# Kernel optimization log

Hardware: AMD Instinct MI355X
Metric: run time of the kernel (lower is better)

## Reference

```python
import jax, jax.numpy as jnp
import numpy as np

B, T, C, H = 4, 4096, 2048, 128  # batch, seq, emb_dim, head_size


def setup_inputs() -> dict:
    key = jax.random.key(0)
    k1, k2, k3, k4 = jax.random.split(key, 4)
    idx = jax.random.normal(k1, (B, T, C), dtype=jnp.float32)
    # nn.Linear weight layout: [out_features, in_features]; scale like torch init
    s = 1.0 / np.sqrt(C)
    Wq = jax.random.uniform(k2, (H, C), jnp.float32, -s, s)
    Wk = jax.random.uniform(k3, (H, C), jnp.float32, -s, s)
    Wv = jax.random.uniform(k4, (H, C), jnp.float32, -s, s)
    return {"idx": idx, "Wq": Wq, "Wk": Wk, "Wv": Wv}


def reference(idx, Wq, Wk, Wv):
    b, t, c = idx.shape
    q = jnp.einsum('btc,hc->bth', idx, Wq)  # [B,T,H]
    k = jnp.einsum('btc,hc->bth', idx, Wk)
    v = jnp.einsum('btc,hc->bth', idx, Wv)
    # NOTE: original computes keys @ queries^T and scales by emb_dim**-0.5
    scale = jnp.asarray(c, idx.dtype) ** -0.5
    wei = jnp.einsum('bih,bjh->bij', k, q) * scale  # [B,T,T]
    causal = jnp.tril(jnp.ones((t, t), dtype=bool))
    wei = jnp.where(causal, wei, -jnp.inf)
    wei = jax.nn.softmax(wei, axis=-1)
    return jnp.einsum('bij,bjh->bih', wei, v)  # [B,T,H]
```

## Files before the change

kernel.cpp:

```cpp
#include <hip/hip_runtime.h>
#include <hip/hip_bf16.h>
#include <cstdint>

#define TSEQ 4096
#define CDIM 2048
#define HDIM 128
#define NCOL 384

typedef short bf8v __attribute__((ext_vector_type(8)));
typedef float f4v  __attribute__((ext_vector_type(4)));

__device__ __forceinline__ unsigned short f2b(float f) {
  union { float f; unsigned u; } v; v.f = f;
  unsigned u = v.u;
  return (unsigned short)((u + 0x7fffu + ((u >> 16) & 1u)) >> 16);
}

__device__ __forceinline__ f4v mfma16(bf8v a, bf8v b, f4v c) {
  return __builtin_amdgcn_mfma_f32_16x16x32_bf16(a, b, c, 0, 0, 0);
}

__global__ void wcat_kernel(const float* __restrict__ Wq, const float* __restrict__ Wk,
                            const float* __restrict__ Wv, unsigned short* __restrict__ Wcat) {
  int e = (blockIdx.x * 256 + threadIdx.x) * 4;
  int n = e >> 11;
  int k = e & 2047;
  const float* src;
  if (n < 128)      src = Wq + (size_t)n * CDIM + k;
  else if (n < 256) src = Wk + (size_t)(n - 128) * CDIM + k;
  else              src = Wv + (size_t)(n - 256) * CDIM + k;
  float4 f = *(const float4*)src;
  ushort4 o;
  o.x = f2b(f.x); o.y = f2b(f.y); o.z = f2b(f.z); o.w = f2b(f.w);
  *(ushort4*)(Wcat + e) = o;
}

__global__ __launch_bounds__(256, 2) void proj_gemm(const float* __restrict__ A,
                                                    const unsigned short* __restrict__ Bw,
                                                    unsigned short* __restrict__ Cq) {
  __shared__ unsigned short As[128][40];
  __shared__ unsigned short Bs[128][40];
  const int m0 = blockIdx.x * 128;
  const int n0 = blockIdx.y * 128;
  const int tid = threadIdx.x;
  const int lane = tid & 63;
  const int w = tid >> 6;
  const int wm = (w & 1) * 64, wn = (w >> 1) * 64;
  const int llo = lane & 15, lhi = lane >> 4;

  f4v acc[4][4];
#pragma unroll
  for (int i = 0; i < 4; ++i)
#pragma unroll
    for (int j = 0; j < 4; ++j) acc[i][j] = (f4v){0.f, 0.f, 0.f, 0.f};

  const int ar = tid >> 3, ac = (tid & 7) * 4;
  const int br = tid >> 2, bc = (tid & 3) * 8;

  for (int k0 = 0; k0 < CDIM; k0 += 32) {
#pragma unroll
    for (int p = 0; p < 4; ++p) {
      int row = p * 32 + ar;
      float4 f = *(const float4*)(A + (size_t)(m0 + row) * CDIM + k0 + ac);
      ushort4 o;
      o.x = f2b(f.x); o.y = f2b(f.y); o.z = f2b(f.z); o.w = f2b(f.w);
      *(ushort4*)&As[row][ac] = o;
    }
#pragma unroll
    for (int p = 0; p < 2; ++p) {
      int row = p * 64 + br;
      *(uint4*)&Bs[row][bc] = *(const uint4*)(Bw + (size_t)(n0 + row) * CDIM + k0 + bc);
    }
    __syncthreads();
    bf8v af[4], bfr[4];
#pragma unroll
    for (int i = 0; i < 4; ++i) af[i]  = *(const bf8v*)&As[wm + i * 16 + llo][lhi * 8];
#pragma unroll
    for (int j = 0; j < 4; ++j) bfr[j] = *(const bf8v*)&Bs[wn + j * 16 + llo][lhi * 8];
#pragma unroll
    for (int i = 0; i < 4; ++i)
#pragma unroll
      for (int j = 0; j < 4; ++j) acc[i][j] = mfma16(af[i], bfr[j], acc[i][j]);
    __syncthreads();
  }
#pragma unroll
  for (int i = 0; i < 4; ++i)
#pragma unroll
    for (int j = 0; j < 4; ++j)
#pragma unroll
      for (int r = 0; r < 4; ++r) {
        int row = m0 + wm + i * 16 + lhi * 4 + r;
        int col = n0 + wn + j * 16 + llo;
        Cq[(size_t)row * NCOL + col] = f2b(acc[i][j][r]);
      }
}

__global__ void pack_frags(const unsigned short* __restrict__ qkv,
                           unsigned short* __restrict__ dst, int colbase) {
  int x = blockIdx.x;
  int b = x >> 8, t16 = x & 255;
  int t = threadIdx.x;
  int kk = t >> 6, lhi = (t >> 4) & 3, llo = t & 15;
  size_t row = (size_t)(b * TSEQ + t16 * 16 + llo);
  bf8v v = *(const bf8v*)(qkv + row * NCOL + colbase + kk * 32 + lhi * 8);
  *(bf8v*)(dst + ((size_t)x * 256 + t) * 8) = v;
}

__global__ void pack_vb(const unsigned short* __restrict__ qkv,
                        unsigned short* __restrict__ VB) {
  __shared__ unsigned short tile[64][136];
  int x = blockIdx.x;
  int b = x >> 6, j64 = x & 63;
  int t = threadIdx.x;
  {
    int r = t >> 2, c = (t & 3) * 32;
    const unsigned short* src = qkv + (size_t)(b * TSEQ + j64 * 64 + r) * NCOL + 256 + c;
    *(uint4*)&tile[r][c]      = *(const uint4*)(src);
    *(uint4*)&tile[r][c + 8]  = *(const uint4*)(src + 8);
    *(uint4*)&tile[r][c + 16] = *(const uint4*)(src + 16);
    *(uint4*)&tile[r][c + 24] = *(const uint4*)(src + 24);
  }
  __syncthreads();
#pragma unroll
  for (int p = 0; p < 4; ++p) {
    int ss = p * 256 + t;
    int jb = ss >> 9, ht = (ss >> 6) & 7, lane = ss & 63;
    int llo = lane & 15, lhi = lane >> 4;
    bf8v v;
#pragma unroll
    for (int e = 0; e < 8; ++e) v[e] = (short)tile[jb * 32 + lhi * 8 + e][ht * 16 + llo];
    *(bf8v*)(VB + (((size_t)(b * 128 + j64 * 2 + jb) * 8 + ht) * 64 + lane) * 8) = v;
  }
}

__global__ __launch_bounds__(256, 4) void attn2(const unsigned short* __restrict__ QB,
                                                const unsigned short* __restrict__ KA,
                                                const unsigned short* __restrict__ VB,
                                                float* __restrict__ out) {
  __shared__ union SM {
    unsigned short Ps[4][16][68];
    struct { float Om[4][16][132]; float Mm[4][16]; float Lm[4][16]; } mg;
  } sm;
  const int x = blockIdx.x;
  const int pair = x >> 1, member = x & 1;
  const int b = pair & 3, sp = pair >> 2;
  const int s = member ? (255 - sp) : sp;
  const int lastjt = s >> 2;
  const int tid = threadIdx.x;
  const int w = tid >> 6, lane = tid & 63;
  const int llo = lane & 15, lhi = lane >> 4;
  const float scale = 0.022097086912079608f;

  bf8v aK[4];
  {
    const unsigned short* kp = KA + (size_t)(b * 256 + s) * 2048;
#pragma unroll
    for (int kk = 0; kk < 4; ++kk) aK[kk] = *(const bf8v*)(kp + (kk * 64 + lane) * 8);
  }

  f4v Oacc[8];
#pragma unroll
  for (int nt = 0; nt < 8; ++nt) Oacc[nt] = (f4v){0.f, 0.f, 0.f, 0.f};
  float mrow[4] = {-3.0e38f, -3.0e38f, -3.0e38f, -3.0e38f};
  float lrow[4] = {0.f, 0.f, 0.f, 0.f};

  for (int jt = w; jt <= lastjt; jt += 4) {
    const unsigned short* qp = QB + (size_t)(b * 256 + jt * 4) * 2048;
    f4v S[4];
#pragma unroll
    for (int ct = 0; ct < 4; ++ct) {
      f4v acc = (f4v){0.f, 0.f, 0.f, 0.f};
#pragma unroll
      for (int kk = 0; kk < 4; ++kk) {
        bf8v bq = *(const bf8v*)(qp + ((ct * 4 + kk) * 64 + lane) * 8);
        acc = mfma16(aK[kk], bq, acc);
      }
      S[ct] = acc * scale;
    }
    if (jt == lastjt) {
#pragma unroll
      for (int ct = 0; ct < 4; ++ct)
#pragma unroll
        for (int r = 0; r < 4; ++r) {
          int j = jt * 64 + ct * 16 + llo;
          int i = s * 16 + lhi * 4 + r;
          if (j > i) S[ct][r] = -3.0e38f;
        }
    }
    float alpha[4];
#pragma unroll
    for (int r = 0; r < 4; ++r) {
      float tm = fmaxf(fmaxf(S[0][r], S[1][r]), fmaxf(S[2][r], S[3][r]));
#pragma unroll
      for (int off = 1; off < 16; off <<= 1) tm = fmaxf(tm, __shfl_xor(tm, off));
      float mn = fmaxf(mrow[r], tm);
      alpha[r] = __expf(mrow[r] - mn);
      mrow[r] = mn;
      float rs = 0.f;
#pragma unroll
      for (int ct = 0; ct < 4; ++ct) {
        float p = __expf(S[ct][r] - mn);
        S[ct][r] = p;
        rs += p;
      }
#pragma unroll
      for (int off = 1; off < 16; off <<= 1) rs += __shfl_xor(rs, off);
      lrow[r] = lrow[r] * alpha[r] + rs;
    }
#pragma unroll
    for (int ct = 0; ct < 4; ++ct)
#pragma unroll
      for (int r = 0; r < 4; ++r)
        sm.Ps[w][lhi * 4 + r][ct * 16 + llo] = f2b(S[ct][r]);
    bf8v aP[2];
#pragma unroll
    for (int kk = 0; kk < 2; ++kk) aP[kk] = *(const bf8v*)&sm.Ps[w][llo][kk * 32 + lhi * 8];
    const unsigned short* vp = VB + (size_t)(b * 128 + jt * 2) * 4096;
#pragma unroll
    for (int nt = 0; nt < 8; ++nt) {
      f4v o = Oacc[nt];
#pragma unroll
      for (int r = 0; r < 4; ++r) o[r] *= alpha[r];
#pragma unroll
      for (int kk = 0; kk < 2; ++kk) {
        bf8v bv = *(const bf8v*)(vp + ((kk * 8 + nt) * 64 + lane) * 8);
        o = mfma16(aP[kk], bv, o);
      }
      Oacc[nt] = o;
    }
  }

  __syncthreads();
#pragma unroll
  for (int nt = 0; nt < 8; ++nt)
#pragma unroll
    for (int r = 0; r < 4; ++r)
      sm.mg.Om[w][lhi * 4 + r][nt * 16 + llo] = Oacc[nt][r];
  if (llo == 0) {
#pragma unroll
    for (int r = 0; r < 4; ++r) {
      sm.mg.Mm[w][lhi * 4 + r] = mrow[r];
      sm.mg.Lm[w][lhi * 4 + r] = lrow[r];
    }
  }
  __syncthreads();
  {
    int row = tid >> 4, c0 = (tid & 15) * 8;
    float m0 = sm.mg.Mm[0][row], m1 = sm.mg.Mm[1][row];
    float m2 = sm.mg.Mm[2][row], m3 = sm.mg.Mm[3][row];
    float M = fmaxf(fmaxf(m0, m1), fmaxf(m2, m3));
    float e0 = __expf(m0 - M), e1 = __expf(m1 - M);
    float e2 = __expf(m2 - M), e3 = __expf(m3 - M);
    float L = sm.mg.Lm[0][row] * e0 + sm.mg.Lm[1][row] * e1 +
              sm.mg.Lm[2][row] * e2 + sm.mg.Lm[3][row] * e3;
    float inv = 1.0f / L;
    float* op = out + (size_t)(b * TSEQ + s * 16 + row) * HDIM + c0;
#pragma unroll
    for (int e = 0; e < 8; ++e) {
      float o = sm.mg.Om[0][row][c0 + e] * e0 + sm.mg.Om[1][row][c0 + e] * e1 +
                sm.mg.Om[2][row][c0 + e] * e2 + sm.mg.Om[3][row][c0 + e] * e3;
      op[e] = o * inv;
    }
  }
}

extern "C" void kernel_launch(void* const* d_in, const int* in_sizes, int n_in,
                              void* d_out, int out_size, void* d_ws, size_t ws_size,
                              hipStream_t stream) {
  const float* idx = (const float*)d_in[0];
  const float* Wq  = (const float*)d_in[1];
  const float* Wk  = (const float*)d_in[2];
  const float* Wv  = (const float*)d_in[3];
  float* out = (float*)d_out;
  char* ws = (char*)d_ws;
  unsigned short* Wcat = (unsigned short*)ws;
  unsigned short* qkv  = (unsigned short*)(ws + ((size_t)2  << 20));
  unsigned short* QB   = (unsigned short*)(ws + ((size_t)16 << 20));
  unsigned short* KA   = (unsigned short*)(ws + ((size_t)21 << 20));
  unsigned short* VB   = (unsigned short*)(ws + ((size_t)26 << 20));

  wcat_kernel<<<768, 256, 0, stream>>>(Wq, Wk, Wv, Wcat);
  proj_gemm<<<dim3(128, 3), 256, 0, stream>>>(idx, Wcat, qkv);
  pack_frags<<<1024, 256, 0, stream>>>(qkv, QB, 0);
  pack_frags<<<1024, 256, 0, stream>>>(qkv, KA, 128);
  pack_vb<<<256, 256, 0, stream>>>(qkv, VB);
  attn2<<<1024, 256, 0, stream>>>(QB, KA, VB, out);
}
```

Baseline: 345.1 us.

## Fuse fragment packing into projection GEMM and widen attention key tiles

```diff
diff --git a/kernel.cpp b/kernel.cpp
--- a/kernel.cpp
+++ b/kernel.cpp
@@ -5,7 +5,6 @@
 #define TSEQ 4096
 #define CDIM 2048
 #define HDIM 128
-#define NCOL 384
 
 typedef short bf8v __attribute__((ext_vector_type(8)));
 typedef float f4v  __attribute__((ext_vector_type(4)));
@@ -37,11 +36,16 @@
 
 __global__ __launch_bounds__(256, 2) void proj_gemm(const float* __restrict__ A,
                                                     const unsigned short* __restrict__ Bw,
-                                                    unsigned short* __restrict__ Cq) {
-  __shared__ unsigned short As[128][40];
-  __shared__ unsigned short Bs[128][40];
+                                                    unsigned short* __restrict__ QB,
+                                                    unsigned short* __restrict__ KA,
+                                                    unsigned short* __restrict__ VB) {
+  __shared__ union {
+    struct { unsigned short As[128][40]; unsigned short Bs[128][40]; } st;
+    unsigned short Ct[128][130];
+  } sm;
   const int m0 = blockIdx.x * 128;
-  const int n0 = blockIdx.y * 128;
+  const int y  = blockIdx.y;
+  const int n0 = y * 128;
   const int tid = threadIdx.x;
   const int lane = tid & 63;
   const int w = tid >> 6;
@@ -64,19 +68,19 @@
       float4 f = *(const float4*)(A + (size_t)(m0 + row) * CDIM + k0 + ac);
       ushort4 o;
       o.x = f2b(f.x); o.y = f2b(f.y); o.z = f2b(f.z); o.w = f2b(f.w);
-      *(ushort4*)&As[row][ac] = o;
+      *(ushort4*)&sm.st.As[row][ac] = o;
     }
 #pragma unroll
     for (int p = 0; p < 2; ++p) {
       int row = p * 64 + br;
-      *(uint4*)&Bs[row][bc] = *(const uint4*)(Bw + (size_t)(n0 + row) * CDIM + k0 + bc);
+      *(uint4*)&sm.st.Bs[row][bc] = *(const uint4*)(Bw + (size_t)(n0 + row) * CDIM + k0 + bc);
     }
     __syncthreads();
     bf8v af[4], bfr[4];
 #pragma unroll
-    for (int i = 0; i < 4; ++i) af[i]  = *(const bf8v*)&As[wm + i * 16 + llo][lhi * 8];
-#pragma unroll
-    for (int j = 0; j < 4; ++j) bfr[j] = *(const bf8v*)&Bs[wn + j * 16 + llo][lhi * 8];
+    for (int i = 0; i < 4; ++i) af[i]  = *(const bf8v*)&sm.st.As[wm + i * 16 + llo][lhi * 8];
+#pragma unroll
+    for (int j = 0; j < 4; ++j) bfr[j] = *(const bf8v*)&sm.st.Bs[wn + j * 16 + llo][lhi * 8];
 #pragma unroll
     for (int i = 0; i < 4; ++i)
 #pragma unroll
@@ -88,64 +92,49 @@
 #pragma unroll
     for (int j = 0; j < 4; ++j)
 #pragma unroll
-      for (int r = 0; r < 4; ++r) {
-        int row = m0 + wm + i * 16 + lhi * 4 + r;
-        int col = n0 + wn + j * 16 + llo;
-        Cq[(size_t)row * NCOL + col] = f2b(acc[i][j][r]);
-      }
-}
-
-__global__ void pack_frags(const unsigned short* __restrict__ qkv,
-                           unsigned short* __restrict__ dst, int colbase) {
-  int x = blockIdx.x;
-  int b = x >> 8, t16 = x & 255;
-  int t = threadIdx.x;
-  int kk = t >> 6, lhi = (t >> 4) & 3, llo = t & 15;
-  size_t row = (size_t)(b * TSEQ + t16 * 16 + llo);
-  bf8v v = *(const bf8v*)(qkv + row * NCOL + colbase + kk * 32 + lhi * 8);
-  *(bf8v*)(dst + ((size_t)x * 256 + t) * 8) = v;
-}
-
-__global__ void pack_vb(const unsigned short* __restrict__ qkv,
-                        unsigned short* __restrict__ VB) {
-  __shared__ unsigned short tile[64][136];
-  int x = blockIdx.x;
-  int b = x >> 6, j64 = x & 63;
-  int t = threadIdx.x;
-  {
-    int r = t >> 2, c = (t & 3) * 32;
-    const unsigned short* src = qkv + (size_t)(b * TSEQ + j64 * 64 + r) * NCOL + 256 + c;
-    *(uint4*)&tile[r][c]      = *(const uint4*)(src);
-    *(uint4*)&tile[r][c + 8]  = *(const uint4*)(src + 8);
-    *(uint4*)&tile[r][c + 16] = *(const uint4*)(src + 16);
-    *(uint4*)&tile[r][c + 24] = *(const uint4*)(src + 24);
-  }
+      for (int r = 0; r < 4; ++r)
+        sm.Ct[wm + i * 16 + lhi * 4 + r][wn + j * 16 + llo] = f2b(acc[i][j][r]);
   __syncthreads();
-#pragma unroll
-  for (int p = 0; p < 4; ++p) {
-    int ss = p * 256 + t;
-    int jb = ss >> 9, ht = (ss >> 6) & 7, lane = ss & 63;
-    int llo = lane & 15, lhi = lane >> 4;
-    bf8v v;
-#pragma unroll
-    for (int e = 0; e < 8; ++e) v[e] = (short)tile[jb * 32 + lhi * 8 + e][ht * 16 + llo];
-    *(bf8v*)(VB + (((size_t)(b * 128 + j64 * 2 + jb) * 8 + ht) * 64 + lane) * 8) = v;
-  }
-}
-
-__global__ __launch_bounds__(256, 4) void attn2(const unsigned short* __restrict__ QB,
+  if (y < 2) {
+    unsigned short* dst = (y == 0) ? QB : KA;
+    const size_t base16 = (size_t)(m0 >> 4);
+#pragma unroll
+    for (int p = 0; p < 8; ++p) {
+      int g = p * 256 + tid;
+      int t16l = g >> 8, kk = (g >> 6) & 3, ln = g & 63;
+      int lo = ln & 15, hi = ln >> 4;
+      bf8v v = *(const bf8v*)&sm.Ct[t16l * 16 + lo][kk * 32 + hi * 8];
+      *(bf8v*)(dst + (((base16 + t16l) * 4 + kk) * 64 + ln) * 8) = v;
+    }
+  } else {
+    const size_t base32 = (size_t)(m0 >> 5);
+#pragma unroll
+    for (int p = 0; p < 8; ++p) {
+      int g = p * 256 + tid;
+      int jbl = g >> 9, ht = (g >> 6) & 7, ln = g & 63;
+      int lo = ln & 15, hi = ln >> 4;
+      bf8v v;
+#pragma unroll
+      for (int e = 0; e < 8; ++e) v[e] = (short)sm.Ct[jbl * 32 + hi * 8 + e][ht * 16 + lo];
+      *(bf8v*)(VB + (((base32 + jbl) * 8 + ht) * 64 + ln) * 8) = v;
+    }
+  }
+}
+
+__global__ __launch_bounds__(256, 4) void attn3(const unsigned short* __restrict__ QB,
                                                 const unsigned short* __restrict__ KA,
                                                 const unsigned short* __restrict__ VB,
                                                 float* __restrict__ out) {
   __shared__ union SM {
-    unsigned short Ps[4][16][68];
-    struct { float Om[4][16][132]; float Mm[4][16]; float Lm[4][16]; } mg;
+    unsigned short Ps[4][16][132];
+    struct { float Om[4][16][66]; float Mm[4][16]; float Lm[4][16]; } mg;
   } sm;
   const int x = blockIdx.x;
-  const int pair = x >> 1, member = x & 1;
-  const int b = pair & 3, sp = pair >> 2;
-  const int s = member ? (255 - sp) : sp;
-  const int lastjt = s >> 2;
+  const int b = x & 3;
+  const int u = x >> 2;
+  const int g = u >> 6, r0 = u & 63;
+  const int s = (g & 1) ? (g * 64 + 63 - r0) : (g * 64 + r0);
+  const int lastjt = s >> 3;
   const int tid = threadIdx.x;
   const int w = tid >> 6, lane = tid & 63;
   const int llo = lane & 15, lhi = lane >> 4;
@@ -165,10 +154,10 @@
   float lrow[4] = {0.f, 0.f, 0.f, 0.f};
 
   for (int jt = w; jt <= lastjt; jt += 4) {
-    const unsigned short* qp = QB + (size_t)(b * 256 + jt * 4) * 2048;
-    f4v S[4];
-#pragma unroll
-    for (int ct = 0; ct < 4; ++ct) {
+    const unsigned short* qp = QB + (size_t)(b * 256 + jt * 8) * 2048;
+    f4v S[8];
+#pragma unroll
+    for (int ct = 0; ct < 8; ++ct) {
       f4v acc = (f4v){0.f, 0.f, 0.f, 0.f};
 #pragma unroll
       for (int kk = 0; kk < 4; ++kk) {
@@ -179,10 +168,10 @@
     }
     if (jt == lastjt) {
 #pragma unroll
-      for (int ct = 0; ct < 4; ++ct)
+      for (int ct = 0; ct < 8; ++ct)
 #pragma unroll
         for (int r = 0; r < 4; ++r) {
-          int j = jt * 64 + ct * 16 + llo;
+          int j = jt * 128 + ct * 16 + llo;
           int i = s * 16 + lhi * 4 + r;
           if (j > i) S[ct][r] = -3.0e38f;
         }
@@ -190,7 +179,9 @@
     float alpha[4];
 #pragma unroll
     for (int r = 0; r < 4; ++r) {
-      float tm = fmaxf(fmaxf(S[0][r], S[1][r]), fmaxf(S[2][r], S[3][r]));
+      float tm = S[0][r];
+#pragma unroll
+      for (int ct = 1; ct < 8; ++ct) tm = fmaxf(tm, S[ct][r]);
 #pragma unroll
       for (int off = 1; off < 16; off <<= 1) tm = fmaxf(tm, __shfl_xor(tm, off));
       float mn = fmaxf(mrow[r], tm);
@@ -198,7 +189,7 @@
       mrow[r] = mn;
       float rs = 0.f;
 #pragma unroll
-      for (int ct = 0; ct < 4; ++ct) {
+      for (int ct = 0; ct < 8; ++ct) {
         float p = __expf(S[ct][r] - mn);
         S[ct][r] = p;
         rs += p;
@@ -208,21 +199,21 @@
       lrow[r] = lrow[r] * alpha[r] + rs;
     }
 #pragma unroll
-    for (int ct = 0; ct < 4; ++ct)
+    for (int ct = 0; ct < 8; ++ct)
 #pragma unroll
       for (int r = 0; r < 4; ++r)
         sm.Ps[w][lhi * 4 + r][ct * 16 + llo] = f2b(S[ct][r]);
-    bf8v aP[2];
-#pragma unroll
-    for (int kk = 0; kk < 2; ++kk) aP[kk] = *(const bf8v*)&sm.Ps[w][llo][kk * 32 + lhi * 8];
-    const unsigned short* vp = VB + (size_t)(b * 128 + jt * 2) * 4096;
+    bf8v aP[4];
+#pragma unroll
+    for (int kk = 0; kk < 4; ++kk) aP[kk] = *(const bf8v*)&sm.Ps[w][llo][kk * 32 + lhi * 8];
+    const unsigned short* vp = VB + (size_t)(b * 128 + jt * 4) * 4096;
 #pragma unroll
     for (int nt = 0; nt < 8; ++nt) {
       f4v o = Oacc[nt];
 #pragma unroll
       for (int r = 0; r < 4; ++r) o[r] *= alpha[r];
 #pragma unroll
-      for (int kk = 0; kk < 2; ++kk) {
+      for (int kk = 0; kk < 4; ++kk) {
         bf8v bv = *(const bf8v*)(vp + ((kk * 8 + nt) * 64 + lane) * 8);
         o = mfma16(aP[kk], bv, o);
       }
@@ -230,36 +221,39 @@
     }
   }
 
-  __syncthreads();
-#pragma unroll
-  for (int nt = 0; nt < 8; ++nt)
-#pragma unroll
-    for (int r = 0; r < 4; ++r)
-      sm.mg.Om[w][lhi * 4 + r][nt * 16 + llo] = Oacc[nt][r];
-  if (llo == 0) {
-#pragma unroll
-    for (int r = 0; r < 4; ++r) {
-      sm.mg.Mm[w][lhi * 4 + r] = mrow[r];
-      sm.mg.Lm[w][lhi * 4 + r] = lrow[r];
-    }
-  }
-  __syncthreads();
-  {
-    int row = tid >> 4, c0 = (tid & 15) * 8;
-    float m0 = sm.mg.Mm[0][row], m1 = sm.mg.Mm[1][row];
-    float m2 = sm.mg.Mm[2][row], m3 = sm.mg.Mm[3][row];
-    float M = fmaxf(fmaxf(m0, m1), fmaxf(m2, m3));
-    float e0 = __expf(m0 - M), e1 = __expf(m1 - M);
-    float e2 = __expf(m2 - M), e3 = __expf(m3 - M);
-    float L = sm.mg.Lm[0][row] * e0 + sm.mg.Lm[1][row] * e1 +
-              sm.mg.Lm[2][row] * e2 + sm.mg.Lm[3][row] * e3;
-    float inv = 1.0f / L;
-    float* op = out + (size_t)(b * TSEQ + s * 16 + row) * HDIM + c0;
-#pragma unroll
-    for (int e = 0; e < 8; ++e) {
-      float o = sm.mg.Om[0][row][c0 + e] * e0 + sm.mg.Om[1][row][c0 + e] * e1 +
-                sm.mg.Om[2][row][c0 + e] * e2 + sm.mg.Om[3][row][c0 + e] * e3;
-      op[e] = o * inv;
+#pragma unroll
+  for (int half = 0; half < 2; ++half) {
+    __syncthreads();
+#pragma unroll
+    for (int nt = 0; nt < 4; ++nt)
+#pragma unroll
+      for (int r = 0; r < 4; ++r)
+        sm.mg.Om[w][lhi * 4 + r][nt * 16 + llo] = Oacc[half * 4 + nt][r];
+    if (half == 0 && llo == 0) {
+#pragma unroll
+      for (int r = 0; r < 4; ++r) {
+        sm.mg.Mm[w][lhi * 4 + r] = mrow[r];
+        sm.mg.Lm[w][lhi * 4 + r] = lrow[r];
+      }
+    }
+    __syncthreads();
+    {
+      int row = tid >> 4, c0 = (tid & 15) * 4;
+      float m0 = sm.mg.Mm[0][row], m1 = sm.mg.Mm[1][row];
+      float m2 = sm.mg.Mm[2][row], m3 = sm.mg.Mm[3][row];
+      float M = fmaxf(fmaxf(m0, m1), fmaxf(m2, m3));
+      float e0 = __expf(m0 - M), e1 = __expf(m1 - M);
+      float e2 = __expf(m2 - M), e3 = __expf(m3 - M);
+      float L = sm.mg.Lm[0][row] * e0 + sm.mg.Lm[1][row] * e1 +
+                sm.mg.Lm[2][row] * e2 + sm.mg.Lm[3][row] * e3;
+      float inv = 1.0f / L;
+      float* op = out + (size_t)(b * TSEQ + s * 16 + row) * HDIM + half * 64 + c0;
+#pragma unroll
+      for (int e = 0; e < 4; ++e) {
+        float o = sm.mg.Om[0][row][c0 + e] * e0 + sm.mg.Om[1][row][c0 + e] * e1 +
+                  sm.mg.Om[2][row][c0 + e] * e2 + sm.mg.Om[3][row][c0 + e] * e3;
+        op[e] = o * inv;
+      }
     }
   }
 }
@@ -274,15 +268,11 @@
   float* out = (float*)d_out;
   char* ws = (char*)d_ws;
   unsigned short* Wcat = (unsigned short*)ws;
-  unsigned short* qkv  = (unsigned short*)(ws + ((size_t)2  << 20));
-  unsigned short* QB   = (unsigned short*)(ws + ((size_t)16 << 20));
-  unsigned short* KA   = (unsigned short*)(ws + ((size_t)21 << 20));
-  unsigned short* VB   = (unsigned short*)(ws + ((size_t)26 << 20));
+  unsigned short* QB   = (unsigned short*)(ws + ((size_t)2  << 20));
+  unsigned short* KA   = (unsigned short*)(ws + ((size_t)7  << 20));
+  unsigned short* VB   = (unsigned short*)(ws + ((size_t)12 << 20));
 
   wcat_kernel<<<768, 256, 0, stream>>>(Wq, Wk, Wv, Wcat);
-  proj_gemm<<<dim3(128, 3), 256, 0, stream>>>(idx, Wcat, qkv);
-  pack_frags<<<1024, 256, 0, stream>>>(qkv, QB, 0);
-  pack_frags<<<1024, 256, 0, stream>>>(qkv, KA, 128);
-  pack_vb<<<256, 256, 0, stream>>>(qkv, VB);
-  attn2<<<1024, 256, 0, stream>>>(QB, KA, VB, out);
-}
+  proj_gemm<<<dim3(128, 3), 256, 0, stream>>>(idx, Wcat, QB, KA, VB);
+  attn3<<<1024, 256, 0, stream>>>(QB, KA, VB, out);
+}
```

After: 455.4 us. +32.0%, slower.
